# Kernel optimization log

Measured on AMD Instinct MI355X. Metric: run time of the kernel, lower is better.

The kernel has to match this reference:

```python
import math
import jax, jax.numpy as jnp
import numpy as np

# Dimensions (scalar irreps: o3.Irreps('8x0e').dim == 8, FullyConnectedTensorProduct
# between scalar irreps reduces to a learned bilinear map with a 3D weight tensor)
N = 50000       # nodes
C = 4           # channel dim ('c' in the einsum 'nci,neio->nceo')
DI = 8          # irreps_in.dim
DE = 8          # irreps_edge_attr.dim (must equal DI for the einsum to typecheck)
DO = 8          # irreps_out.dim (must equal DI for lin2 to consume the messages)
DA = 16         # irreps_node_attr.dim
E = 400000      # edges
F_EDGE = 32     # number_of_edge_features
H = 64          # radial_neurons
NUM_NEIGHBORS = 8


def setup_inputs() -> dict:
    key = jax.random.key(0)
    ks = jax.random.split(key, 12)
    inv = lambda f: 1.0 / np.sqrt(f)
    return {
        "node_input": jax.random.normal(ks[0], (N, C, DI), jnp.float32),
        "node_attr": jax.random.normal(ks[1], (N, DA), jnp.float32),
        "edge_features": jax.random.normal(ks[2], (E, F_EDGE), jnp.float32),
        # bilinear tensor-product weights (sc, lin1, lin2)
        "W_sc": jax.random.normal(ks[3], (DI, DA, DO), jnp.float32) * inv(DI * DA),
        "W_lin1": jax.random.normal(ks[4], (DI, DA, DI), jnp.float32) * inv(DI * DA),
        "W_lin2": jax.random.normal(ks[5], (DO, DA, DO), jnp.float32) * inv(DO * DA),
        # radial MLP: Linear(F_EDGE,H) -> SiLU -> Linear(H, DI*DE*DO)
        "fc_w1": jax.random.normal(ks[6], (F_EDGE, H), jnp.float32) * inv(F_EDGE),
        "fc_b1": jnp.zeros((H,), jnp.float32),
        "fc_w2": jax.random.normal(ks[7], (H, DI * DE * DO), jnp.float32) * inv(H),
        "fc_b2": jnp.zeros((DI * DE * DO,), jnp.float32),
        "edge_src": jax.random.randint(ks[8], (E,), 0, N, jnp.int32),
        "edge_dst": jax.random.randint(ks[9], (E,), 0, N, jnp.int32),
    }


def reference(node_input, node_attr, edge_features, W_sc, W_lin1, W_lin2,
              fc_w1, fc_b1, fc_w2, fc_b2, edge_src, edge_dst):
    n_nodes = node_input.shape[0]
    # self-connection and input linear (bilinear in node feature & node attr)
    s = jnp.einsum('nci,na,iao->nco', node_input, node_attr, W_sc)      # [N,C,DO]
    x = jnp.einsum('nci,na,iaj->ncj', node_input, node_attr, W_lin1)    # [N,C,DI]
    # radial MLP -> per-edge weight tensor [E, DI, DE, DO]
    h = jax.nn.silu(edge_features @ fc_w1 + fc_b1)
    ef = (h @ fc_w2 + fc_b2).reshape(-1, DI, DE, DO)
    # gather by source, per-edge contraction (einsum 'nci,neio->nceo'):
    # contract x's irrep dim with ef axis 2, keep ef axis 1 as output dim d
    msg = jnp.einsum('eci,edio->ecdo', x[edge_src], ef)                 # [E,C,DI,DO]
    # scatter-add to destination nodes
    agg = jax.ops.segment_sum(msg, edge_dst, num_segments=n_nodes)      # [N,C,DI,DO]
    agg = agg / jnp.sqrt(jnp.asarray(NUM_NEIGHBORS, agg.dtype))
    # output linear on the last (irreps_out) axis
    x2 = jnp.einsum('ncdo,na,oap->ncdp', agg, node_attr, W_lin2)        # [N,C,DI,DO]
    c_s = math.sin(math.pi / 8.0)
    # fully-connected scalar-irrep TP -> output_mask is all ones -> c_x scalar
    c_x = math.cos(math.pi / 8.0)
    return c_s * s[:, :, None, :] + c_x * x2
```

## Files before the change

### kernel.cpp

```cpp
#include <hip/hip_runtime.h>
#include <math.h>

#define CC 4
#define FE 32
#define HH 64
#define EBS 256
#define KEXT 544
#define ASTR 69

typedef __attribute__((ext_vector_type(8))) short bf16x8;
typedef __attribute__((ext_vector_type(4))) float f32x4;

__device__ inline unsigned short f2bf(float f) {
    unsigned u = __float_as_uint(f);
    u += 0x7fffu + ((u >> 16) & 1u);
    return (unsigned short)(u >> 16);
}
__device__ inline float bf2f(unsigned short b) {
    return __uint_as_float(((unsigned)b) << 16);
}

__global__ __launch_bounds__(256) void k_nodeprep(
    const float* __restrict__ node_input, const float* __restrict__ node_attr,
    const float* __restrict__ W_lin1, const float* __restrict__ W_sc,
    const float* __restrict__ W_lin2,
    float* __restrict__ xbuf, float* __restrict__ sbuf,
    float* __restrict__ w2n_ws, int N)
{
    const float c_s = 0.3826834323650898f;
    const float c_x_scaled = 0.9238795325112867f * 0.35355339059327373f;
    int node = blockIdx.x * 4 + (threadIdx.x >> 6);
    int lane = threadIdx.x & 63;
    if (node >= N) return;

    float attr_own = (lane < 16) ? node_attr[(size_t)node * 16 + lane] : 0.f;
    float ni_own   = (lane < 32) ? node_input[(size_t)node * 32 + lane] : 0.f;

    int iw = lane >> 3, jw = lane & 7;
    float wb1 = 0.f, wbs = 0.f, w2n = 0.f;
    #pragma unroll
    for (int a = 0; a < 16; ++a) {
        float fa = __shfl(attr_own, a);
        int idx = (iw * 16 + a) * 8 + jw;
        wb1 += fa * W_lin1[idx];
        wbs += fa * W_sc[idx];
        w2n += fa * W_lin2[idx];
    }
    w2n_ws[(size_t)node * 64 + lane] = c_x_scaled * w2n;

    int c_ = (lane >> 3) & 3, jo = lane & 7;
    float xo = 0.f, so = 0.f;
    #pragma unroll
    for (int i = 0; i < 8; ++i) {
        float niv = __shfl(ni_own, c_ * 8 + i);
        xo += niv * __shfl(wb1, i * 8 + jo);
        so += niv * __shfl(wbs, i * 8 + jo);
    }
    if (lane < 32) {
        xbuf[(size_t)node * 32 + lane] = xo;
        sbuf[(size_t)node * 32 + lane] = c_s * so;
    }
}

__global__ __launch_bounds__(256) void k_hist(
    const int* __restrict__ edge_dst, int* __restrict__ counts, int E)
{
    int e = blockIdx.x * 256 + threadIdx.x;
    if (e < E) atomicAdd(&counts[edge_dst[e]], 1);
}

__global__ __launch_bounds__(1024) void k_scanA(
    const int* __restrict__ counts, int* __restrict__ offsets,
    int* __restrict__ btot, int N)
{
    __shared__ int wsum[16];
    __shared__ int wpre[16];
    int tid = threadIdx.x, wid = tid >> 6, lane = tid & 63;
    int idx = blockIdx.x * 1024 + tid;
    int v = (idx < N) ? counts[idx] : 0;
    int x = v;
    #pragma unroll
    for (int s = 1; s < 64; s <<= 1) {
        int y = __shfl_up(x, s);
        if (lane >= s) x += y;
    }
    if (lane == 63) wsum[wid] = x;
    __syncthreads();
    if (wid == 0) {
        int wv = (lane < 16) ? wsum[lane] : 0;
        int wx = wv;
        #pragma unroll
        for (int s = 1; s < 16; s <<= 1) {
            int y = __shfl_up(wx, s);
            if (lane >= s) wx += y;
        }
        if (lane < 16) wpre[lane] = wx - wv;
    }
    __syncthreads();
    int excl = wpre[wid] + (x - v);
    if (idx < N) offsets[idx] = excl;
    if (tid == 1023) btot[blockIdx.x] = excl + v;
}

__global__ __launch_bounds__(1024) void k_scanB(int* __restrict__ btot, int nb)
{
    __shared__ int wsum[16];
    __shared__ int wpre[16];
    int tid = threadIdx.x, wid = tid >> 6, lane = tid & 63;
    int v = (tid < nb) ? btot[tid] : 0;
    int x = v;
    #pragma unroll
    for (int s = 1; s < 64; s <<= 1) {
        int y = __shfl_up(x, s);
        if (lane >= s) x += y;
    }
    if (lane == 63) wsum[wid] = x;
    __syncthreads();
    if (wid == 0) {
        int wv = (lane < 16) ? wsum[lane] : 0;
        int wx = wv;
        #pragma unroll
        for (int s = 1; s < 16; s <<= 1) {
            int y = __shfl_up(wx, s);
            if (lane >= s) wx += y;
        }
        if (lane < 16) wpre[lane] = wx - wv;
    }
    __syncthreads();
    if (tid < nb) btot[tid] = wpre[wid] + (x - v);
}

__global__ __launch_bounds__(256) void k_scanC(
    int* __restrict__ offsets, const int* __restrict__ btot,
    int* __restrict__ cursor, int N)
{
    int i = blockIdx.x * 256 + threadIdx.x;
    if (i < N) {
        int o = offsets[i] + btot[i >> 10];
        offsets[i] = o;
        cursor[i] = o;
    }
}

__global__ __launch_bounds__(256) void k_fill(
    const int* __restrict__ edge_dst, const int* __restrict__ edge_src,
    int* __restrict__ cursor, int2* __restrict__ esrc, int E)
{
    int e = blockIdx.x * 256 + threadIdx.x;
    if (e < E) {
        int pos = atomicAdd(&cursor[edge_dst[e]], 1);
        int2 v; v.x = e; v.y = edge_src[e];
        esrc[pos] = v;
    }
}

__global__ __launch_bounds__(256) void k_prep_bfrag(
    const float* __restrict__ fc_w2, const float* __restrict__ fc_b2,
    unsigned short* __restrict__ Bfrag)
{
    int t = blockIdx.x * 256 + threadIdx.x;
    if (t >= KEXT * 64) return;
    int kappa = t >> 6, nu = t & 63;
    int d = nu >> 3, o = nu & 7;
    float val;
    if (kappa < 512)      val = fc_w2[(size_t)(kappa >> 3) * 512 + d * 64 + (kappa & 7) * 8 + o];
    else if (kappa < 520) val = fc_b2[d * 64 + (kappa & 7) * 8 + o];
    else                  val = 0.f;
    int kk = kappa >> 5;
    int lane = ((kappa >> 3) & 3) * 16 + (nu & 15);
    int ct = nu >> 4;
    int j = kappa & 7;
    Bfrag[(size_t)((kk * 4 + ct) * 64 + lane) * 8 + j] = f2bf(val);
}

__global__ __launch_bounds__(256) void k_prep_bfrag1(
    const float* __restrict__ fc_w1, unsigned short* __restrict__ Bfrag1)
{
    int t = blockIdx.x * 256 + threadIdx.x;
    if (t >= 4 * 64 * 8) return;
    int j = t & 7, l = (t >> 3) & 63, ct = t >> 9;
    int k = (l >> 4) * 8 + j;
    int n = ct * 16 + (l & 15);
    Bfrag1[t] = f2bf(fc_w1[(size_t)k * HH + n]);
}

__global__ __launch_bounds__(256) void k_hsilu(
    const float* __restrict__ edge_features,
    const unsigned short* __restrict__ Bfrag1, const float* __restrict__ fc_b1,
    unsigned short* __restrict__ H, int E)
{
    int wid = threadIdx.x >> 6, lane = threadIdx.x & 63;
    int e0 = (blockIdx.x * 4 + wid) * 16;
    if (e0 >= E) return;

    bf16x8 b[4];
    #pragma unroll
    for (int ct = 0; ct < 4; ++ct) {
        uint4 bv = reinterpret_cast<const uint4*>(Bfrag1)[ct * 64 + lane];
        b[ct] = *reinterpret_cast<bf16x8*>(&bv);
    }
    float bias[4];
    #pragma unroll
    for (int ct = 0; ct < 4; ++ct) bias[ct] = fc_b1[ct * 16 + (lane & 15)];

    int row = e0 + (lane & 15);
    if (row >= E) row = E - 1;
    const float4* ap = reinterpret_cast<const float4*>(
        edge_features + (size_t)row * FE + (lane >> 4) * 8);
    float4 a0 = ap[0], a1 = ap[1];
    unsigned au[4];
    au[0] = (unsigned)f2bf(a0.x) | ((unsigned)f2bf(a0.y) << 16);
    au[1] = (unsigned)f2bf(a0.z) | ((unsigned)f2bf(a0.w) << 16);
    au[2] = (unsigned)f2bf(a1.x) | ((unsigned)f2bf(a1.y) << 16);
    au[3] = (unsigned)f2bf(a1.z) | ((unsigned)f2bf(a1.w) << 16);
    bf16x8 a = *reinterpret_cast<bf16x8*>(au);

    f32x4 acc[4];
    #pragma unroll
    for (int ct = 0; ct < 4; ++ct) {
        acc[ct] = (f32x4){0.f, 0.f, 0.f, 0.f};
        acc[ct] = __builtin_amdgcn_mfma_f32_16x16x32_bf16(a, b[ct], acc[ct], 0, 0, 0);
    }

    #pragma unroll
    for (int ct = 0; ct < 4; ++ct) {
        #pragma unroll
        for (int v = 0; v < 4; ++v) {
            int r = e0 + (lane >> 4) * 4 + v;
            if (r < E) {
                float x = acc[ct][v] + bias[ct];
                float s = x / (1.f + __expf(-x));
                H[(size_t)r * HH + ct * 16 + (lane & 15)] = f2bf(s);
            }
        }
    }
}

__global__ __launch_bounds__(256) void k_zgemm(
    const unsigned short* __restrict__ H, const int2* __restrict__ esrc,
    const int* __restrict__ offsets, const int* __restrict__ counts,
    const float* __restrict__ xin, const unsigned short* __restrict__ Bfrag,
    const float* __restrict__ sbuf, const float* __restrict__ w2n_ws,
    float* __restrict__ out, int N)
{
    __shared__ uint4 alds[16 * ASTR];
    int wid = threadIdx.x >> 6, lane = threadIdx.x & 63;
    int node = blockIdx.x * 4 + wid;
    bool valid = (node < N);

    float z[CC][8];
    #pragma unroll
    for (int c = 0; c < CC; ++c)
        #pragma unroll
        for (int i = 0; i < 8; ++i) z[c][i] = 0.f;
    float xsown = 0.f;

    int off = 0, cnt = 0;
    if (valid) { off = offsets[node]; cnt = counts[node]; }
    for (int base = 0; base < cnt; base += 64) {
        int m = (cnt - base < 64) ? (cnt - base) : 64;
        int2 ej = (lane < m) ? esrc[off + base + lane] : make_int2(0, 0);
        for (int cb = 0; cb < m; cb += 8) {
            int mm = m - cb; if (mm > 8) mm = 8;
            float hk[8];
            int   ssrc[8];
            #pragma unroll
            for (int t = 0; t < 8; ++t) {
                int jj = cb + (t < mm ? t : 0);
                int e  = __shfl(ej.x, jj);
                ssrc[t] = __builtin_amdgcn_readfirstlane(__shfl(ej.y, jj));
                hk[t]  = bf2f(H[(size_t)e * HH + lane]);
            }
            #pragma unroll
            for (int t = 0; t < 8; ++t) {
                if (t < mm) {
                    const float* xr = xin + (size_t)ssrc[t] * 32;
                    float h = hk[t];
                    #pragma unroll
                    for (int c = 0; c < CC; ++c)
                        #pragma unroll
                        for (int i = 0; i < 8; ++i)
                            z[c][i] += h * xr[c * 8 + i];
                    xsown += xin[(size_t)ssrc[t] * 32 + (lane & 31)];
                }
            }
        }
    }

    #pragma unroll
    for (int c = 0; c < CC; ++c) {
        uint4 pk;
        pk.x = (unsigned)f2bf(z[c][0]) | ((unsigned)f2bf(z[c][1]) << 16);
        pk.y = (unsigned)f2bf(z[c][2]) | ((unsigned)f2bf(z[c][3]) << 16);
        pk.z = (unsigned)f2bf(z[c][4]) | ((unsigned)f2bf(z[c][5]) << 16);
        pk.w = (unsigned)f2bf(z[c][6]) | ((unsigned)f2bf(z[c][7]) << 16);
        alds[(wid * 4 + c) * ASTR + lane] = pk;
    }
    float xb[8];
    #pragma unroll
    for (int i = 0; i < 8; ++i) xb[i] = __shfl(xsown, (lane & 3) * 8 + i);
    int r4 = wid * 4;
    if (lane < 4) {
        uint4 pk;
        pk.x = (unsigned)f2bf(xb[0]) | ((unsigned)f2bf(xb[1]) << 16);
        pk.y = (unsigned)f2bf(xb[2]) | ((unsigned)f2bf(xb[3]) << 16);
        pk.z = (unsigned)f2bf(xb[4]) | ((unsigned)f2bf(xb[5]) << 16);
        pk.w = (unsigned)f2bf(xb[6]) | ((unsigned)f2bf(xb[7]) << 16);
        alds[(r4 + lane) * ASTR + 64] = pk;
    } else if (lane < 16) {
        int j = lane - 4;
        uint4 zz; zz.x = 0u; zz.y = 0u; zz.z = 0u; zz.w = 0u;
        alds[(r4 + (j & 3)) * ASTR + 65 + (j >> 2)] = zz;
    }

    bf16x8 bfr[17];
    #pragma unroll
    for (int kk = 0; kk < 16; ++kk) {
        uint4 bv = reinterpret_cast<const uint4*>(Bfrag)[(kk * 4 + wid) * 64 + lane];
        bfr[kk] = *reinterpret_cast<bf16x8*>(&bv);
    }
    {
        uint4 bv = reinterpret_cast<const uint4*>(Bfrag)[(64 + wid) * 64 + lane];
        bfr[16] = *reinterpret_cast<bf16x8*>(&bv);
    }

    __syncthreads();

    f32x4 acc = (f32x4){0.f, 0.f, 0.f, 0.f};
    #pragma unroll
    for (int kk = 0; kk < 16; ++kk) {
        uint4 av = alds[(lane & 15) * ASTR + kk * 4 + (lane >> 4)];
        bf16x8 a = *reinterpret_cast<bf16x8*>(&av);
        acc = __builtin_amdgcn_mfma_f32_16x16x32_bf16(a, bfr[kk], acc, 0, 0, 0);
    }
    {
        uint4 av = alds[(lane & 15) * ASTR + 64 + (lane >> 4)];
        bf16x8 a = *reinterpret_cast<bf16x8*>(&av);
        acc = __builtin_amdgcn_mfma_f32_16x16x32_bf16(a, bfr[16], acc, 0, 0, 0);
    }

    int q = lane >> 4;
    int colc = lane & 15;
    int nq = blockIdx.x * 4 + q;
    bool vq = (nq < N);
    int realn = vq ? nq : 0;
    int col = wid * 16 + colc;
    int p = col & 7;
    int dloc8 = (colc >> 3) << 3;
    float w2r[8];
    #pragma unroll
    for (int o = 0; o < 8; ++o)
        w2r[o] = vq ? w2n_ws[(size_t)realn * 64 + o * 8 + p] : 0.f;
    #pragma unroll
    for (int v = 0; v < 4; ++v) {
        float res = 0.f;
        #pragma unroll
        for (int o = 0; o < 8; ++o)
            res += __shfl(acc[v], q * 16 + dloc8 + o) * w2r[o];
        if (vq) {
            float sv = sbuf[(size_t)realn * 32 + v * 8 + p];
            out[(size_t)(realn * 4 + v) * 64 + col] = sv + res;
        }
    }
}

__global__ __launch_bounds__(256) void k_node_out(
    const float* __restrict__ sbuf, const float* __restrict__ w2n_ws,
    float* __restrict__ out, int N)
{
    int node = blockIdx.x * 4 + (threadIdx.x >> 6);
    int lane = threadIdx.x & 63;
    if (node >= N) return;
    int d = lane >> 3, p = lane & 7;

    float w2 = w2n_ws[(size_t)node * 64 + lane];
    float s_own = sbuf[(size_t)node * 32 + (lane & 31)];

    float w2sh[8];
    #pragma unroll
    for (int o = 0; o < 8; ++o) w2sh[o] = __shfl(w2, o * 8 + p);

    float* rowp = out + (size_t)node * 256;
    #pragma unroll
    for (int c = 0; c < CC; ++c) {
        float a_own = rowp[c * 64 + lane];
        float res = 0.f;
        #pragma unroll
        for (int o = 0; o < 8; ++o)
            res += __shfl(a_own, d * 8 + o) * w2sh[o];
        float sval = __shfl(s_own, c * 8 + p);
        rowp[c * 64 + lane] = sval + res;
    }
}

__global__ __launch_bounds__(EBS) void k_edge_atomic(
    const float* __restrict__ edge_features,
    const float* __restrict__ fc_w1, const float* __restrict__ fc_b1,
    const float* __restrict__ fc_w2, const float* __restrict__ fc_b2,
    const int* __restrict__ edge_src, const int* __restrict__ edge_dst,
    const float* __restrict__ xin, float* __restrict__ agg, int E)
{
    __shared__ float hlds[HH * EBS];
    int e = blockIdx.x * EBS + threadIdx.x;
    if (e >= E) return;
    float h[HH];
    #pragma unroll
    for (int k = 0; k < HH; ++k) h[k] = fc_b1[k];
    const float4* efp = reinterpret_cast<const float4*>(edge_features + (size_t)e * FE);
    #pragma unroll
    for (int fq = 0; fq < FE / 4; ++fq) {
        float4 efv = efp[fq];
        float ev[4] = {efv.x, efv.y, efv.z, efv.w};
        #pragma unroll
        for (int fs = 0; fs < 4; ++fs) {
            float evv = ev[fs];
            const float4* w1p = reinterpret_cast<const float4*>(fc_w1 + (fq * 4 + fs) * HH);
            #pragma unroll
            for (int q = 0; q < HH / 4; ++q) {
                float4 w = w1p[q];
                h[q * 4 + 0] += evv * w.x;
                h[q * 4 + 1] += evv * w.y;
                h[q * 4 + 2] += evv * w.z;
                h[q * 4 + 3] += evv * w.w;
            }
        }
    }
    #pragma unroll
    for (int k = 0; k < HH; ++k) {
        float v = h[k];
        hlds[k * EBS + threadIdx.x] = v / (1.f + __expf(-v));
    }
    int src = edge_src[e], dst = edge_dst[e];
    float xs[32];
    const float4* xp = reinterpret_cast<const float4*>(xin + (size_t)src * 32);
    #pragma unroll
    for (int q = 0; q < 8; ++q) {
        float4 v = xp[q];
        xs[q * 4 + 0] = v.x; xs[q * 4 + 1] = v.y;
        xs[q * 4 + 2] = v.z; xs[q * 4 + 3] = v.w;
    }
    float* outp = agg + (size_t)dst * 256;
    #pragma unroll 1
    for (int d = 0; d < 8; ++d) {
        float t[64];
        const float4* b2p = reinterpret_cast<const float4*>(fc_b2 + d * 64);
        #pragma unroll
        for (int q = 0; q < 16; ++q) {
            float4 v = b2p[q];
            t[q * 4 + 0] = v.x; t[q * 4 + 1] = v.y;
            t[q * 4 + 2] = v.z; t[q * 4 + 3] = v.w;
        }
        for (int k = 0; k < HH; ++k) {
            float hv = hlds[k * EBS + threadIdx.x];
            const float4* wp = reinterpret_cast<const float4*>(fc_w2 + (size_t)k * 512 + d * 64);
            #pragma unroll
            for (int q = 0; q < 16; ++q) {
                float4 w = wp[q];
                t[q * 4 + 0] += hv * w.x;
                t[q * 4 + 1] += hv * w.y;
                t[q * 4 + 2] += hv * w.z;
                t[q * 4 + 3] += hv * w.w;
            }
        }
        #pragma unroll
        for (int c = 0; c < CC; ++c) {
            #pragma unroll
            for (int o = 0; o < 8; ++o) {
                float acc = 0.f;
                #pragma unroll
                for (int i = 0; i < 8; ++i) acc += xs[c * 8 + i] * t[i * 8 + o];
                atomicAdd(outp + c * 64 + d * 8 + o, acc);
            }
        }
    }
}

extern "C" void kernel_launch(void* const* d_in, const int* in_sizes, int n_in,
                              void* d_out, int out_size, void* d_ws, size_t ws_size,
                              hipStream_t stream)
{
    const float* node_input    = (const float*)d_in[0];
    const float* node_attr     = (const float*)d_in[1];
    const float* edge_features = (const float*)d_in[2];
    const float* W_sc          = (const float*)d_in[3];
    const float* W_lin1        = (const float*)d_in[4];
    const float* W_lin2        = (const float*)d_in[5];
    const float* fc_w1         = (const float*)d_in[6];
    const float* fc_b1         = (const float*)d_in[7];
    const float* fc_w2         = (const float*)d_in[8];
    const float* fc_b2         = (const float*)d_in[9];
    const int*   edge_src      = (const int*)d_in[10];
    const int*   edge_dst      = (const int*)d_in[11];

    const int N = in_sizes[1] / 16;
    const int E = in_sizes[10];
    const int nb = (N + 1023) / 1024;

    char* ws = (char*)d_ws;
    size_t off = 0;
    auto take = [&](size_t bytes) { char* p = ws + off; off += (bytes + 15) & ~(size_t)15; return p; };
    float* xbuf            = (float*)take((size_t)N * 32 * sizeof(float));
    float* sbuf            = (float*)take((size_t)N * 32 * sizeof(float));
    float* w2n_ws          = (float*)take((size_t)N * 64 * sizeof(float));
    int*   counts          = (int*)take((size_t)N * sizeof(int));
    int*   offsets         = (int*)take((size_t)N * sizeof(int));
    int*   cursor          = (int*)take((size_t)N * sizeof(int));
    int*   btot            = (int*)take((size_t)1024 * sizeof(int));
    int2*  esrc            = (int2*)take((size_t)E * sizeof(int2));
    unsigned short* Bfrag  = (unsigned short*)take((size_t)17 * 4 * 64 * 8 * sizeof(unsigned short));
    unsigned short* Bfrag1 = (unsigned short*)take((size_t)4 * 64 * 8 * sizeof(unsigned short));
    unsigned short* Hbuf   = (unsigned short*)take((size_t)E * HH * sizeof(unsigned short));
    bool fast = (off <= ws_size);

    float* out = (float*)d_out;

    k_nodeprep<<<(N + 3) / 4, 256, 0, stream>>>(
        node_input, node_attr, W_lin1, W_sc, W_lin2, xbuf, sbuf, w2n_ws, N);

    if (fast) {
        hipMemsetAsync(counts, 0, (size_t)N * sizeof(int), stream);
        k_hist<<<(E + 255) / 256, 256, 0, stream>>>(edge_dst, counts, E);
        k_scanA<<<nb, 1024, 0, stream>>>(counts, offsets, btot, N);
        k_scanB<<<1, 1024, 0, stream>>>(btot, nb);
        k_scanC<<<(N + 255) / 256, 256, 0, stream>>>(offsets, btot, cursor, N);
        k_fill<<<(E + 255) / 256, 256, 0, stream>>>(edge_dst, edge_src, cursor, esrc, E);
        k_prep_bfrag1<<<(4 * 64 * 8 + 255) / 256, 256, 0, stream>>>(fc_w1, Bfrag1);
        k_prep_bfrag<<<(KEXT * 64 + 255) / 256, 256, 0, stream>>>(fc_w2, fc_b2, Bfrag);
        k_hsilu<<<(E + 63) / 64, 256, 0, stream>>>(edge_features, Bfrag1, fc_b1, Hbuf, E);
        k_zgemm<<<(N + 3) / 4, 256, 0, stream>>>(
            Hbuf, esrc, offsets, counts, xbuf, Bfrag, sbuf, w2n_ws, out, N);
    } else {
        hipMemsetAsync(d_out, 0, (size_t)out_size * sizeof(float), stream);
        k_edge_atomic<<<(E + EBS - 1) / EBS, EBS, 0, stream>>>(
            edge_features, fc_w1, fc_b1, fc_w2, fc_b2, edge_src, edge_dst, xbuf, out, E);
        k_node_out<<<(N + 3) / 4, 256, 0, stream>>>(sbuf, w2n_ws, out, N);
    }
}
```

Baseline: 284.3 us.

## Write hidden activations in CSR edge order and stream them contiguously

The fill kernel now records each edge's sorted position, and the hidden-layer kernel scatters its bf16 SiLU outputs directly into destination-sorted order. The aggregation kernel then reads H rows contiguously per node instead of gathering by original edge id, and loads x rows as float4 vectors. It also replaces the 8-edge batched gather loop with a simple per-edge loop unrolled by two. This trades scattered 128-byte writes in k_hsilu for sequential reads in k_zgemm, and the simpler loop may expose less memory-level parallelism.

New measurement: 289.8 us. Within noise of the previous version (+1.9%).

```diff
diff --git a/kernel.cpp b/kernel.cpp
--- a/kernel.cpp
+++ b/kernel.cpp
@@ -144,13 +144,13 @@
 
 __global__ __launch_bounds__(256) void k_fill(
     const int* __restrict__ edge_dst, const int* __restrict__ edge_src,
-    int* __restrict__ cursor, int2* __restrict__ esrc, int E)
+    int* __restrict__ cursor, int* __restrict__ srcs, int* __restrict__ epos, int E)
 {
     int e = blockIdx.x * 256 + threadIdx.x;
     if (e < E) {
         int pos = atomicAdd(&cursor[edge_dst[e]], 1);
-        int2 v; v.x = e; v.y = edge_src[e];
-        esrc[pos] = v;
+        srcs[pos] = edge_src[e];
+        epos[e] = pos;
     }
 }
 
@@ -187,6 +187,7 @@
 __global__ __launch_bounds__(256) void k_hsilu(
     const float* __restrict__ edge_features,
     const unsigned short* __restrict__ Bfrag1, const float* __restrict__ fc_b1,
+    const int* __restrict__ epos,
     unsigned short* __restrict__ H, int E)
 {
     int wid = threadIdx.x >> 6, lane = threadIdx.x & 63;
@@ -202,6 +203,13 @@
     float bias[4];
     #pragma unroll
     for (int ct = 0; ct < 4; ++ct) bias[ct] = fc_b1[ct * 16 + (lane & 15)];
+
+    int pr[4];
+    #pragma unroll
+    for (int v = 0; v < 4; ++v) {
+        int r = e0 + (lane >> 4) * 4 + v;
+        pr[v] = (r < E) ? epos[r] : -1;
+    }
 
     int row = e0 + (lane & 15);
     if (row >= E) row = E - 1;
@@ -226,18 +234,17 @@
     for (int ct = 0; ct < 4; ++ct) {
         #pragma unroll
         for (int v = 0; v < 4; ++v) {
-            int r = e0 + (lane >> 4) * 4 + v;
-            if (r < E) {
+            if (pr[v] >= 0) {
                 float x = acc[ct][v] + bias[ct];
                 float s = x / (1.f + __expf(-x));
-                H[(size_t)r * HH + ct * 16 + (lane & 15)] = f2bf(s);
+                H[(size_t)pr[v] * HH + ct * 16 + (lane & 15)] = f2bf(s);
             }
         }
     }
 }
 
 __global__ __launch_bounds__(256) void k_zgemm(
-    const unsigned short* __restrict__ H, const int2* __restrict__ esrc,
+    const unsigned short* __restrict__ H, const int* __restrict__ srcs,
     const int* __restrict__ offsets, const int* __restrict__ counts,
     const float* __restrict__ xin, const unsigned short* __restrict__ Bfrag,
     const float* __restrict__ sbuf, const float* __restrict__ w2n_ws,
@@ -259,31 +266,25 @@
     if (valid) { off = offsets[node]; cnt = counts[node]; }
     for (int base = 0; base < cnt; base += 64) {
         int m = (cnt - base < 64) ? (cnt - base) : 64;
-        int2 ej = (lane < m) ? esrc[off + base + lane] : make_int2(0, 0);
-        for (int cb = 0; cb < m; cb += 8) {
-            int mm = m - cb; if (mm > 8) mm = 8;
-            float hk[8];
-            int   ssrc[8];
+        int sj = (lane < m) ? srcs[off + base + lane] : 0;
+        #pragma unroll 2
+        for (int j = 0; j < m; ++j) {
+            int src = __shfl(sj, j);
+            float hk = bf2f(H[(size_t)(off + base + j) * HH + lane]);
+            const float4* xp = reinterpret_cast<const float4*>(xin + (size_t)src * 32);
+            float xs[32];
             #pragma unroll
-            for (int t = 0; t < 8; ++t) {
-                int jj = cb + (t < mm ? t : 0);
-                int e  = __shfl(ej.x, jj);
-                ssrc[t] = __builtin_amdgcn_readfirstlane(__shfl(ej.y, jj));
-                hk[t]  = bf2f(H[(size_t)e * HH + lane]);
+            for (int q = 0; q < 8; ++q) {
+                float4 v = xp[q];
+                xs[q * 4 + 0] = v.x; xs[q * 4 + 1] = v.y;
+                xs[q * 4 + 2] = v.z; xs[q * 4 + 3] = v.w;
             }
             #pragma unroll
-            for (int t = 0; t < 8; ++t) {
-                if (t < mm) {
-                    const float* xr = xin + (size_t)ssrc[t] * 32;
-                    float h = hk[t];
-                    #pragma unroll
-                    for (int c = 0; c < CC; ++c)
-                        #pragma unroll
-                        for (int i = 0; i < 8; ++i)
-                            z[c][i] += h * xr[c * 8 + i];
-                    xsown += xin[(size_t)ssrc[t] * 32 + (lane & 31)];
-                }
-            }
+            for (int c = 0; c < CC; ++c)
+                #pragma unroll
+                for (int i = 0; i < 8; ++i)
+                    z[c][i] += hk * xs[c * 8 + i];
+            xsown += xin[(size_t)src * 32 + (lane & 31)];
         }
     }
 
@@ -506,7 +507,8 @@
     int*   offsets         = (int*)take((size_t)N * sizeof(int));
     int*   cursor          = (int*)take((size_t)N * sizeof(int));
     int*   btot            = (int*)take((size_t)1024 * sizeof(int));
-    int2*  esrc            = (int2*)take((size_t)E * sizeof(int2));
+    int*   srcs            = (int*)take((size_t)E * sizeof(int));
+    int*   epos            = (int*)take((size_t)E * sizeof(int));
     unsigned short* Bfrag  = (unsigned short*)take((size_t)17 * 4 * 64 * 8 * sizeof(unsigned short));
     unsigned short* Bfrag1 = (unsigned short*)take((size_t)4 * 64 * 8 * sizeof(unsigned short));
     unsigned short* Hbuf   = (unsigned short*)take((size_t)E * HH * sizeof(unsigned short));
@@ -523,12 +525,12 @@
         k_scanA<<<nb, 1024, 0, stream>>>(counts, offsets, btot, N);
         k_scanB<<<1, 1024, 0, stream>>>(btot, nb);
         k_scanC<<<(N + 255) / 256, 256, 0, stream>>>(offsets, btot, cursor, N);
-        k_fill<<<(E + 255) / 256, 256, 0, stream>>>(edge_dst, edge_src, cursor, esrc, E);
+        k_fill<<<(E + 255) / 256, 256, 0, stream>>>(edge_dst, edge_src, cursor, srcs, epos, E);
         k_prep_bfrag1<<<(4 * 64 * 8 + 255) / 256, 256, 0, stream>>>(fc_w1, Bfrag1);
         k_prep_bfrag<<<(KEXT * 64 + 255) / 256, 256, 0, stream>>>(fc_w2, fc_b2, Bfrag);
-        k_hsilu<<<(E + 63) / 64, 256, 0, stream>>>(edge_features, Bfrag1, fc_b1, Hbuf, E);
+        k_hsilu<<<(E + 63) / 64, 256, 0, stream>>>(edge_features, Bfrag1, fc_b1, epos, Hbuf, E);
         k_zgemm<<<(N + 3) / 4, 256, 0, stream>>>(
-            Hbuf, esrc, offsets, counts, xbuf, Bfrag, sbuf, w2n_ws, out, N);
+            Hbuf, srcs, offsets, counts, xbuf, Bfrag, sbuf, w2n_ws, out, N);
     } else {
         hipMemsetAsync(d_out, 0, (size_t)out_size * sizeof(float), stream);
         k_edge_atomic<<<(E + EBS - 1) / EBS, EBS, 0, stream>>>(
```
